# Optimization experiments

Measured on AMD Instinct MI355X. Metric: run time of the kernel, lower is better.

## Reference

```python
import jax, jax.numpy as jnp
import numpy as np

_COUNTS = [256, 192, 128, 64]


def _l2norm(x, axis=1):
    # F.normalize(p=2): x / max(||x||, eps)
    return x / jnp.maximum(jnp.linalg.norm(x, axis=axis, keepdims=True), 1e-12)


def _gcn(x, w1, b1, w2, b2, w3, b3):
    # stack of kernel-size-1 Conv1d == channel matmuls; x: [B, C, N]
    h = jax.nn.relu(jnp.einsum('oc,bcn->bon', w1, x) + b1[:, None])
    h = jax.nn.relu(jnp.einsum('oc,bcn->bon', w2, h) + b2[:, None])
    return jnp.einsum('oc,bcn->bon', w3, h) + b3[:, None]


def setup_inputs() -> dict:
    key = jax.random.key(0)
    ks = iter(jax.random.split(key, 64))
    feat_shapes = [(8, 256, 100, 100), (8, 512, 50, 50), (8, 1024, 25, 25), (8, 2048, 13, 13)]
    chans = [256, 512, 1024, 2048]
    C = 256
    d = {}
    for i, s in enumerate(feat_shapes):
        d[f'feat{i}'] = jax.random.normal(next(ks), s, jnp.float32)
    for i, (ci, ni) in enumerate(zip(chans, _COUNTS)):
        d[f'w_sem_{i}'] = jax.random.normal(next(ks), (ni, ci), jnp.float32) * 0.02
        d[f'w_emb_{i}'] = jax.random.normal(next(ks), (C, ci), jnp.float32) * 0.02
        d[f'w_q_{i}'] = jax.random.normal(next(ks), (C, ci), jnp.float32) * 0.02
        d[f'w_out_{i}'] = jax.random.normal(next(ks), (C, C), jnp.float32) * 0.02
        d[f'w_res_{i}'] = jax.random.normal(next(ks), (C, ci), jnp.float32) * 0.02
    d['gw1'] = jax.random.normal(next(ks), (4, 64, C), jnp.float32) * 0.05
    d['gb1'] = jnp.zeros((4, 64), jnp.float32)
    d['gw2'] = jax.random.normal(next(ks), (4, 64, 64), jnp.float32) * 0.05
    d['gb2'] = jnp.zeros((4, 64), jnp.float32)
    d['gw3'] = jax.random.normal(next(ks), (4, C, 64), jnp.float32) * 0.05
    d['gb3'] = jnp.zeros((4, C), jnp.float32)
    d['mw1'] = jax.random.normal(next(ks), (64, C), jnp.float32) * 0.05
    d['mb1'] = jnp.zeros((64,), jnp.float32)
    d['mw2'] = jax.random.normal(next(ks), (64, 64), jnp.float32) * 0.05
    d['mb2'] = jnp.zeros((64,), jnp.float32)
    d['mw3'] = jax.random.normal(next(ks), (C, 64), jnp.float32) * 0.05
    d['mb3'] = jnp.zeros((C,), jnp.float32)
    return d


def reference(feat0, feat1, feat2, feat3,
              w_sem_0, w_sem_1, w_sem_2, w_sem_3,
              w_emb_0, w_emb_1, w_emb_2, w_emb_3,
              w_q_0, w_q_1, w_q_2, w_q_3,
              w_out_0, w_out_1, w_out_2, w_out_3,
              w_res_0, w_res_1, w_res_2, w_res_3,
              gw1, gb1, gw2, gb2, gw3, gb3,
              mw1, mb1, mw2, mb2, mw3, mb3):
    feats = [feat0, feat1, feat2, feat3]
    w_sem = [w_sem_0, w_sem_1, w_sem_2, w_sem_3]
    w_emb = [w_emb_0, w_emb_1, w_emb_2, w_emb_3]
    w_q = [w_q_0, w_q_1, w_q_2, w_q_3]
    w_out = [w_out_0, w_out_1, w_out_2, w_out_3]
    w_res = [w_res_0, w_res_1, w_res_2, w_res_3]

    # ---- context collector ----
    contexts = []
    for i in range(4):
        f = feats[i]
        B, ci, H, W = f.shape
        hw = H * W
        sem = jnp.einsum('nc,bchw->bnhw', w_sem[i], f)                 # [B, ni, H, W]
        emb = jnp.einsum('oc,bchw->bohw', w_emb[i], f).reshape(B, -1, hw)  # [B, C, HW]
        fn = _l2norm(f, 1).reshape(B, ci, hw)
        en = _l2norm(sem, 1).reshape(B, -1, hw)
        # torch.einsum('bni,bci->bni') sums over c -> entities * sum_c(features)
        sim = en * fn.sum(axis=1, keepdims=True) * jnp.sqrt(jnp.float32(ci))
        attn = jax.nn.softmax(sim, axis=2)                              # softmax over HW
        contexts.append(jnp.einsum('bop,bnp->bon', emb, attn))          # [B, C, ni]

    # ---- graph reasoning ----
    refined = [_gcn(c, gw1[i], gb1[i], gw2[i], gb2[i], gw3[i], gb3[i]) + c
               for i, c in enumerate(contexts)]
    g = jnp.concatenate(refined, axis=2)                                # [B, C, 640]
    g = _gcn(g, mw1, mb1, mw2, mb2, mw3, mb3) + g

    # ---- context distributor ----
    outs = []
    ptr = 0
    for i in range(4):
        f = feats[i]
        B, ci, H, W = f.shape
        hw = H * W
        ni = _COUNTS[i]
        lc = g[:, :, ptr:ptr + ni]                                      # [B, C, ni]
        ptr += ni
        q = jnp.einsum('oc,bchw->bohw', w_q[i], f).reshape(B, -1, hw)   # [B, C, HW]
        scores = jnp.einsum('bop,bon->bpn', _l2norm(q, 1), _l2norm(lc, 1))  # [B, HW, ni]
        aw = jax.nn.softmax(scores, axis=2)                             # softmax over ni
        wc = jnp.einsum('bon,bpn->bop', lc, aw).reshape(B, -1, H, W)    # [B, C, H, W]
        out = jnp.einsum('oc,bchw->bohw', w_out[i], wc) + jnp.einsum('oc,bchw->bohw', w_res[i], f)
        outs.append(out)
    return tuple(outs)
```

## Files before the change

### kernel.cpp

```cpp
#include <hip/hip_runtime.h>
#include <math.h>


#define BB 8
#define CC 256
#define GG 640

typedef __attribute__((ext_vector_type(8))) short short8;
typedef __attribute__((ext_vector_type(4))) float f32x4;

__device__ __forceinline__ unsigned short f2bf(float f) {
    unsigned int u = __float_as_uint(f);
    u += 0x7fffu + ((u >> 16) & 1u);
    return (unsigned short)(u >> 16);
}
__device__ __forceinline__ float bf2f(unsigned short h) {
    return __uint_as_float(((unsigned int)h) << 16);
}
__device__ __forceinline__ float h2f(unsigned short h) {
    union { unsigned short u; _Float16 x; } cv; cv.u = h; return (float)cv.x;
}
__device__ __forceinline__ unsigned short f2h(float f) {
    union { unsigned short u; _Float16 x; } cv; cv.x = (_Float16)f; return cv.u;
}

__device__ __forceinline__ void glds16(const unsigned short* g, unsigned short* l) {
    __builtin_amdgcn_global_load_lds(
        (const __attribute__((address_space(1))) void*)g,
        (__attribute__((address_space(3))) void*)l, 16, 0, 0);
}

__device__ __forceinline__ int swz(int row, int seg) { return seg ^ ((row >> 1) & 3); }

__global__ __launch_bounds__(256) void mfmaGemm(
    const unsigned short* __restrict__ A, long sA, int lda,
    const unsigned short* __restrict__ B, long sB, int ldb,
    const unsigned short* __restrict__ B2p, long sB2, int ldb2, int Kb,
    void* __restrict__ C, long sC, int ldc, long offC,
    int M, int N, int K, int kChunks, int kChunkLen, int mode,
    int gxn, int gym,
    void* __restrict__ C2, long sC2, int ldc2, long offC2, int M1, int mode2)
{
    __shared__ __align__(16) unsigned short As[2][128 * 32];
    __shared__ __align__(16) unsigned short Bs[2][128 * 32];

    const int nb = (int)gridDim.x;
    int orig = (int)blockIdx.x;
    int xcd = orig & 7, idx = orig >> 3;
    int q8 = nb >> 3, r8 = nb & 7;
    int wg = (xcd < r8) ? (xcd * (q8 + 1) + idx)
                        : (r8 * (q8 + 1) + (xcd - r8) * q8 + idx);
    int mb, nbk, z;
    if (N >= M) { mb = wg % gym; int t = wg / gym; nbk = t % gxn; z = t / gxn; }
    else        { nbk = wg % gxn; int t = wg / gxn; mb = t % gym; z = t / gym; }

    const int b = z / kChunks, chunk = z - b * kChunks;
    const int kbeg = chunk * kChunkLen;
    const int kend = min(K, kbeg + kChunkLen);
    const int m0 = mb * 128, n0 = nbk * 128;

    const unsigned short* Ab  = A + (long)b * sA;
    const unsigned short* Bb  = B + (long)b * sB;
    const unsigned short* Bb2 = B2p ? (B2p + (long)b * sB2) : nullptr;

    const int tid = threadIdx.x;
    const int row = tid >> 2, seg = tid & 3;
    const int wave = tid >> 6, lane = tid & 63;
    const int wm = (wave & 1) * 64, wn = (wave >> 1) * 64;
    const int lm = lane & 15, kq = lane >> 4;

    const bool okA  = ((lda  & 7) == 0) && ((((size_t)Ab)  & 15) == 0);
    const bool okB  = ((ldb  & 7) == 0) && ((((size_t)Bb)  & 15) == 0);
    const bool okB2 = Bb2 && ((ldb2 & 7) == 0) && ((((size_t)Bb2) & 15) == 0);

    f32x4 acc[4][4];
    #pragma unroll
    for (int i = 0; i < 4; ++i)
        #pragma unroll
        for (int j = 0; j < 4; ++j) acc[i][j] = (f32x4){0.f, 0.f, 0.f, 0.f};

    auto stageF = [&](const unsigned short* Pb, int ld, int o0,
                      unsigned short* LS, int kg) {
        #pragma unroll
        for (int l = 0; l < 2; ++l) {
            int rf = l * 64 + row;
            const unsigned short* src = Pb + (long)(o0 + rf) * ld + kg + swz(rf, seg) * 8;
            glds16(src, &LS[rf * 32 + seg * 8]);
        }
    };
    auto stageS = [&](const unsigned short* Pb, int ld, int lim, int o0,
                      unsigned short* LS, int kg, int lend) {
        #pragma unroll
        for (int l = 0; l < 2; ++l) {
            int rf = l * 64 + row;
            int kgg = kg + swz(rf, seg) * 8;
            int krem = lend - kgg;
            int g = o0 + rf;
            uint4 v = make_uint4(0u, 0u, 0u, 0u);
            if (g < lim && krem > 0) {
                const unsigned short* src = Pb + (long)g * ld + kgg;
                if (krem >= 8 && ((((size_t)src) & 15) == 0)) {
                    v = *(const uint4*)src;
                } else {
                    __align__(16) unsigned short tmp[8] = {0,0,0,0,0,0,0,0};
                    int c = krem < 8 ? krem : 8;
                    for (int j = 0; j < c; ++j) tmp[j] = src[j];
                    v = *(const uint4*)tmp;
                }
            }
            *(uint4*)&LS[rf * 32 + seg * 8] = v;
        }
    };
    auto stage = [&](int kg, int buf) {
        bool full = (kg + 32 <= kend);
        if (okA && full) stageF(Ab, lda, m0, As[buf], kg);
        else             stageS(Ab, lda, M, m0, As[buf], kg, kend);
        if (kg < Kb) {
            if (okB && full) stageF(Bb, ldb, n0, Bs[buf], kg);
            else             stageS(Bb, ldb, N, n0, Bs[buf], kg, min(kend, Kb));
        } else {
            int kl = kg - Kb;
            if (okB2 && full) stageF(Bb2, ldb2, n0, Bs[buf], kl);
            else              stageS(Bb2, ldb2, N, n0, Bs[buf], kl, kend - Kb);
        }
    };

    stage(kbeg, 0);
    int cur = 0;
    for (int k0 = kbeg; k0 < kend; k0 += 32) {
        __syncthreads();
        if (k0 + 32 < kend) stage(k0 + 32, cur ^ 1);

        short8 af[4], bfr[4];
        #pragma unroll
        for (int mt = 0; mt < 4; ++mt) {
            int rA = wm + mt * 16 + lm;
            af[mt] = *(const short8*)&As[cur][rA * 32 + swz(rA, kq) * 8];
        }
        #pragma unroll
        for (int nt = 0; nt < 4; ++nt) {
            int rB = wn + nt * 16 + lm;
            bfr[nt] = *(const short8*)&Bs[cur][rB * 32 + swz(rB, kq) * 8];
        }
        #pragma unroll
        for (int mt = 0; mt < 4; ++mt)
            #pragma unroll
            for (int nt = 0; nt < 4; ++nt)
                acc[mt][nt] = __builtin_amdgcn_mfma_f32_16x16x32_bf16(
                    af[mt], bfr[nt], acc[mt][nt], 0, 0, 0);
        cur ^= 1;
    }

    const long cb1 = (long)b * sC + offC;
    const long cb2 = (long)b * sC2 + offC2;
    #pragma unroll
    for (int mt = 0; mt < 4; ++mt) {
        #pragma unroll
        for (int nt = 0; nt < 4; ++nt) {
            int n_g = n0 + wn + nt * 16 + lm;
            if (n_g >= N) continue;
            #pragma unroll
            for (int r = 0; r < 4; ++r) {
                int m_g = m0 + wm + mt * 16 + kq * 4 + r;
                if (m_g >= M) continue;
                float v = acc[mt][nt][r];
                void* Cp; int md; long cix;
                if (m_g < M1) { Cp = C;  md = mode;  cix = cb1 + (long)m_g * ldc + n_g; }
                else          { Cp = C2; md = mode2; cix = cb2 + (long)(m_g - M1) * ldc2 + n_g; }
                if (md == 0)      ((float*)Cp)[cix] = v;
                else if (md == 1) ((float*)Cp)[cix] += v;
                else if (md == 2) atomicAdd(&((float*)Cp)[cix], v);
                else if (md == 3) ((unsigned short*)Cp)[cix] = f2h(v);
                else              ((unsigned short*)Cp)[cix] = f2bf(v);
            }
        }
    }
}

__global__ __launch_bounds__(256) void gemmA(
    const float* __restrict__ W, long sW,
    const float* __restrict__ X, long sX, int ldx, long offX,
    float* __restrict__ Cd, long sC, int ldc, long offC,
    const float* __restrict__ bias,
    const float* __restrict__ res, long sR, int ldr, long offR,
    int O, int K, int P, int relu, int accum,
    int lvlFuse, long wStride, int bStride)
{
    __shared__ float Ws[16][64];
    __shared__ float Xs[16][64];
    const int tid = threadIdx.x;
    const int tx = tid & 15;
    const int ty = tid >> 4;
    const int b  = blockIdx.z;
    const int o0 = blockIdx.y * 64;
    const int p0 = blockIdx.x * 64;

    const float* Wp = W;
    const float* bp = bias;
    if (lvlFuse) {
        int lvl = p0 >= 576 ? 3 : p0 >= 448 ? 2 : p0 >= 256 ? 1 : 0;
        Wp += (long)lvl * wStride;
        if (bias) bp += (long)lvl * bStride;
    }
    const float* Wb = Wp + (long)b * sW;
    const float* Xb = X + (long)b * sX + offX;

    float acc[4][4] = {};

    const int wo = tid >> 2;
    const int wk = (tid & 3) * 4;
    const int xp = tid & 63;
    const int xq = tid >> 6;

    for (int k0 = 0; k0 < K; k0 += 16) {
        #pragma unroll
        for (int u = 0; u < 4; ++u) {
            int kk = wk + u;
            float v = 0.f;
            if (o0 + wo < O && k0 + kk < K) v = Wb[(long)(o0 + wo) * K + k0 + kk];
            Ws[kk][wo] = v;
        }
        #pragma unroll
        for (int u = 0; u < 4; ++u) {
            int kk = xq * 4 + u;
            float v = 0.f;
            if (p0 + xp < P && k0 + kk < K) v = Xb[(long)(k0 + kk) * ldx + (p0 + xp)];
            Xs[kk][xp] = v;
        }
        __syncthreads();
        #pragma unroll
        for (int kk = 0; kk < 16; ++kk) {
            float4 wv = *(const float4*)&Ws[kk][ty * 4];
            float4 xv = *(const float4*)&Xs[kk][tx * 4];
            float wa[4] = {wv.x, wv.y, wv.z, wv.w};
            float xa[4] = {xv.x, xv.y, xv.z, xv.w};
            #pragma unroll
            for (int i = 0; i < 4; ++i)
                #pragma unroll
                for (int j = 0; j < 4; ++j)
                    acc[i][j] += wa[i] * xa[j];
        }
        __syncthreads();
    }

    #pragma unroll
    for (int i = 0; i < 4; ++i) {
        int o = o0 + ty * 4 + i;
        if (o >= O) continue;
        #pragma unroll
        for (int j = 0; j < 4; ++j) {
            int p = p0 + tx * 4 + j;
            if (p >= P) continue;
            float v = acc[i][j];
            if (bias) v += bp[o];
            if (relu) v = fmaxf(v, 0.f);
            if (res)  v += res[(long)b * sR + offR + (long)o * ldr + p];
            long ci_ = (long)b * sC + offC + (long)o * ldc + p;
            if (accum) Cd[ci_] += v; else Cd[ci_] = v;
        }
    }
}

__global__ __launch_bounds__(256) void transCvtF(
    const float* __restrict__ src, long sS, int R, int Cc,
    unsigned short* __restrict__ dst, long sD,
    const float* __restrict__ scale, long sScale)
{
    __shared__ float tile[32][33];
    int b = blockIdx.z;
    int r0 = blockIdx.y * 32, c0 = blockIdx.x * 32;
    const float* sb = src + (long)b * sS;
    unsigned short* db = dst + (long)b * sD;
    int tr = threadIdx.x >> 5, tc = threadIdx.x & 31;
    #pragma unroll
    for (int it = 0; it < 4; ++it) {
        int r = r0 + tr + it * 8, c = c0 + tc;
        tile[tr + it * 8][tc] = (r < R && c < Cc) ? sb[(long)r * Cc + c] : 0.f;
    }
    __syncthreads();
    #pragma unroll
    for (int it = 0; it < 4; ++it) {
        int c = c0 + tr + it * 8;
        int r = r0 + tc;
        if (c < Cc && r < R) {
            float v = tile[tc][tr + it * 8];
            if (scale) v *= scale[(long)b * sScale + c];
            db[(long)c * R + r] = f2bf(v);
        }
    }
}

__global__ __launch_bounds__(256) void transCvtH(
    const unsigned short* __restrict__ src, long sS, int R, int Cc,
    unsigned short* __restrict__ dst, long sD,
    const float* __restrict__ scale, long sScale)
{
    __shared__ float tile[32][33];
    int b = blockIdx.z;
    int r0 = blockIdx.y * 32, c0 = blockIdx.x * 32;
    const unsigned short* sb = src + (long)b * sS;
    unsigned short* db = dst + (long)b * sD;
    int tr = threadIdx.x >> 5, tc = threadIdx.x & 31;
    #pragma unroll
    for (int it = 0; it < 4; ++it) {
        int r = r0 + tr + it * 8, c = c0 + tc;
        tile[tr + it * 8][tc] = (r < R && c < Cc) ? h2f(sb[(long)r * Cc + c]) : 0.f;
    }
    __syncthreads();
    #pragma unroll
    for (int it = 0; it < 4; ++it) {
        int c = c0 + tr + it * 8;
        int r = r0 + tc;
        if (c < Cc && r < R) {
            float v = tile[tc][tr + it * 8];
            if (scale) v *= scale[(long)b * sScale + c];
            db[(long)c * R + r] = f2bf(v);
        }
    }
}

__global__ __launch_bounds__(256) void posStatsT(
    const unsigned short* __restrict__ featT, float* __restrict__ fscale,
    int ci, int hw, float sq)
{
    int b = blockIdx.y, p = blockIdx.x;
    const unsigned short* row = featT + ((long)b * hw + p) * ci;
    float s = 0.f, ss = 0.f;
    for (int c = threadIdx.x; c < ci; c += 256) {
        float v = bf2f(row[c]); s += v; ss += v * v;
    }
    __shared__ float rs[256], rss[256];
    int tid = threadIdx.x;
    rs[tid] = s; rss[tid] = ss; __syncthreads();
    for (int st = 128; st > 0; st >>= 1) {
        if (tid < st) { rs[tid] += rs[tid + st]; rss[tid] += rss[tid + st]; }
        __syncthreads();
    }
    if (tid == 0)
        fscale[(long)b * hw + p] = rs[0] / fmaxf(sqrtf(rss[0]), 1e-12f) * sq;
}

__global__ void enScale(const unsigned short* __restrict__ sem, float* __restrict__ fscale,
                        int ni, int hw)
{
    int b = blockIdx.y;
    int p = blockIdx.x * 256 + threadIdx.x;
    if (p >= hw) return;
    const unsigned short* sb = sem + (long)b * ni * hw + p;
    float ss = 0.f;
    for (int n = 0; n < ni; ++n) { float v = h2f(sb[(long)n * hw]); ss += v * v; }
    fscale[(long)b * hw + p] = fscale[(long)b * hw + p] / fmaxf(sqrtf(ss), 1e-12f);
}

__global__ __launch_bounds__(256) void softmaxHW(
    unsigned short* buf, const float* __restrict__ scale, int ni, int hw)
{
    int b = blockIdx.y, n = blockIdx.x;
    unsigned short* row = buf + ((long)b * ni + n) * hw;
    const float* sc = scale + (long)b * hw;
    __shared__ float red[256];
    int tid = threadIdx.x;

    float m = -1e30f;
    for (int p = tid; p < hw; p += 256) m = fmaxf(m, h2f(row[p]) * sc[p]);
    red[tid] = m; __syncthreads();
    for (int s = 128; s > 0; s >>= 1) {
        if (tid < s) red[tid] = fmaxf(red[tid], red[tid + s]);
        __syncthreads();
    }
    m = red[0]; __syncthreads();

    float sum = 0.f;
    for (int p = tid; p < hw; p += 256) sum += __expf(h2f(row[p]) * sc[p] - m);
    red[tid] = sum; __syncthreads();
    for (int s = 128; s > 0; s >>= 1) {
        if (tid < s) red[tid] += red[tid + s];
        __syncthreads();
    }
    float inv = 1.0f / red[0];

    for (int p = tid; p < hw; p += 256) {
        float v = __expf(h2f(row[p]) * sc[p] - m) * inv;
        row[p] = f2bf(v);
    }
}

__global__ void softmaxN(unsigned short* buf, int hw, int ni)
{
    int b = blockIdx.y;
    int wav = threadIdx.x >> 6, lane = threadIdx.x & 63;
    int p = blockIdx.x * 4 + wav;
    if (p >= hw) return;
    unsigned short* row = buf + ((long)b * hw + p) * ni;
    float m = -1e30f;
    for (int n = lane; n < ni; n += 64) m = fmaxf(m, h2f(row[n]));
    for (int off = 32; off > 0; off >>= 1) m = fmaxf(m, __shfl_xor(m, off));
    float s = 0.f;
    for (int n = lane; n < ni; n += 64) s += __expf(h2f(row[n]) - m);
    for (int off = 32; off > 0; off >>= 1) s += __shfl_xor(s, off);
    float inv = 1.f / s;
    for (int n = lane; n < ni; n += 64) {
        float v = __expf(h2f(row[n]) - m) * inv;
        row[n] = f2bf(v);
    }
}

__global__ void lcRnorm(const float* __restrict__ g2, float* __restrict__ lcr)
{
    int b = blockIdx.y;
    int col = blockIdx.x * 256 + threadIdx.x;
    if (col >= GG) return;
    const float* gb = g2 + (long)b * CC * GG + col;
    float ss = 0.f;
    for (int o = 0; o < CC; ++o) { float v = gb[o * GG]; ss += v * v; }
    lcr[b * GG + col] = 1.f / fmaxf(sqrtf(ss), 1e-12f);
}

__global__ void buildLc(const float* __restrict__ g2, const float* __restrict__ lcr,
                        unsigned short* __restrict__ lcnT, unsigned short* __restrict__ lcB,
                        int ni, int ptr)
{
    long t = (long)blockIdx.x * 256 + threadIdx.x;
    if (t >= (long)BB * ni * CC) return;
    int o = (int)(t & (CC - 1));
    long r = t >> 8;
    int n = (int)(r % ni);
    int b = (int)(r / ni);
    float raw = g2[(long)b * CC * GG + (long)o * GG + ptr + n];
    lcnT[t] = f2bf(raw * lcr[b * GG + ptr + n]);
    lcB[((long)b * CC + o) * ni + n] = f2bf(raw);
}

__global__ void qNormCol(const unsigned short* __restrict__ q, float* __restrict__ scl, int hw)
{
    int b = blockIdx.y;
    int p = blockIdx.x * 256 + threadIdx.x;
    if (p >= hw) return;
    const unsigned short* qb = q + (long)b * CC * hw + p;
    float ss = 0.f;
    for (int o = 0; o < CC; ++o) { float v = h2f(qb[(long)o * hw]); ss += v * v; }
    scl[(long)b * hw + p] = 1.f / fmaxf(sqrtf(ss), 1e-12f);
}

struct CvtJob { const float* src; long off; int n; int K; int ld; int colOff; };
struct CvtJobs { CvtJob j[20]; };
__global__ void cvtAllK(CvtJobs jobs, unsigned short* __restrict__ dst)
{
    const CvtJob J = jobs.j[blockIdx.y];
    int t = blockIdx.x * 256 + threadIdx.x;
    if (t < J.n) {
        int r = t / J.K, c = t - r * J.K;
        dst[J.off + (long)r * J.ld + J.colOff + c] = f2bf(J.src[t]);
    }
}

__global__ void cvtOut(const float* __restrict__ src, unsigned short* __restrict__ dst,
                       int n, int toF16)
{
    int i = blockIdx.x * 256 + threadIdx.x;
    if (i >= n) return;
    float v = src[i];
    dst[i] = toF16 ? f2h(v) : f2bf(v);
}

extern "C" void kernel_launch(void* const* d_in, const int* in_sizes, int n_in,
                              void* d_out, int out_size, void* d_ws, size_t ws_size,
                              hipStream_t stream)
{
    (void)n_in; (void)out_size;
    static const int  CI[4]  = {256, 512, 1024, 2048};
    static const int  NI[4]  = {256, 192, 128, 64};
    static const int  HWs[4] = {10000, 2500, 625, 169};
    static const int  PTR[4] = {0, 256, 448, 576};
    static const long OUTOFF[4] = {0, 20480000L, 25600000L, 26880000L};

    const float* feat[4];
    for (int i = 0; i < 4; ++i) feat[i] = (const float*)d_in[i];

    const float *w_sem[4], *w_emb[4], *w_q[4], *w_out[4], *w_res[4];
    bool grouped = (in_sizes[5] == 192 * 512);
    for (int i = 0; i < 4; ++i) {
        if (grouped) {
            w_sem[i] = (const float*)d_in[4 + i];
            w_emb[i] = (const float*)d_in[8 + i];
            w_q[i]   = (const float*)d_in[12 + i];
            w_out[i] = (const float*)d_in[16 + i];
            w_res[i] = (const float*)d_in[20 + i];
        } else {
            int base = 4 + 5 * i;
            w_sem[i] = (const float*)d_in[base + 0];
            w_emb[i] = (const float*)d_in[base + 1];
            w_q[i]   = (const float*)d_in[base + 2];
            w_out[i] = (const float*)d_in[base + 3];
            w_res[i] = (const float*)d_in[base + 4];
        }
    }
    const float* gw1 = (const float*)d_in[24];
    const float* gb1 = (const float*)d_in[25];
    const float* gw2 = (const float*)d_in[26];
    const float* gb2 = (const float*)d_in[27];
    const float* gw3 = (const float*)d_in[28];
    const float* gb3 = (const float*)d_in[29];
    const float* mw1 = (const float*)d_in[30];
    const float* mb1 = (const float*)d_in[31];
    const float* mw2 = (const float*)d_in[32];
    const float* mb2 = (const float*)d_in[33];
    const float* mw3 = (const float*)d_in[34];
    const float* mb3 = (const float*)d_in[35];

    char* wp = (char*)d_ws;
    auto carve = [&](size_t bytes) { char* r = wp; wp += (bytes + 255) & ~(size_t)255; return r; };
    unsigned short* R1 = (unsigned short*)carve(40960000);
    unsigned short* R2 = (unsigned short*)carve(40960000);
    unsigned short* R3 = (unsigned short*)carve(40960000);
    float* ctxg = (float*)carve(5242880);
    float* gbuf = (float*)carve(5242880);
    float* g2   = (float*)carve(5242880);
    float* h1   = (float*)carve(1310720);
    float* h2   = (float*)carve(1310720);
    unsigned short* lcnT = (unsigned short*)carve(1048576);
    unsigned short* lcB  = (unsigned short*)carve(1048576);
    float* lcr  = (float*)carve(20480);
    float* scl  = (float*)carve(320000);
    float* SK   = (float*)carve(5120000);
    unsigned short* wbuf = (unsigned short*)carve(7500000);

    unsigned short* featP[4];
    featP[0] = R1;
    {
        size_t f1 = 2UL * BB * 2500 * 512;
        size_t f2 = 2UL * BB * 625 * 1024;
        size_t f3 = 2UL * BB * 169 * 2048;
        size_t used = (size_t)(wp - (char*)d_ws);
        bool ok = (used + f1 + f2 + f3 + (1u << 20) + 4096) <= ws_size;
        if (ok) {
            featP[1] = (unsigned short*)carve(f1);
            featP[2] = (unsigned short*)carve(f2);
            featP[3] = (unsigned short*)carve(f3);
            carve(1u << 20);
        } else {
            featP[1] = featP[2] = featP[3] = R1;
        }
    }
    bool persist = (featP[1] != R1);

    float* outp = (float*)d_out;

    CvtJobs jobs;
    unsigned short *wsemB[4], *wqB[4], *woutresB[4];
    long woff = 0; int maxn = 0, jx = 0;
    auto addJob = [&](const float* s, int n, int K, int ld, int colOff, long off) {
        jobs.j[jx].src = s; jobs.j[jx].off = off; jobs.j[jx].n = n;
        jobs.j[jx].K = K; jobs.j[jx].ld = ld; jobs.j[jx].colOff = colOff;
        if (n > maxn) maxn = n;
        ++jx;
    };
    for (int i = 0; i < 4; ++i) {
        int ci = CI[i], ni = NI[i];
        wsemB[i] = wbuf + woff;
        addJob(w_sem[i], ni * ci, ci, ci, 0, woff);  woff += ni * ci;
        addJob(w_emb[i], CC * ci, ci, ci, 0, woff);  woff += CC * ci;
        wqB[i] = wbuf + woff;
        addJob(w_q[i],   CC * ci, ci, ci, 0, woff);  woff += CC * ci;
        woutresB[i] = wbuf + woff;
        addJob(w_out[i], CC * CC, CC, CC + ci, 0,  woff);
        addJob(w_res[i], CC * ci, ci, CC + ci, CC, woff);
        woff += (long)CC * (CC + ci);
    }

    cvtAllK<<<dim3((maxn + 255) / 256, 20), 256, 0, stream>>>(jobs, wbuf);

    auto mgFull = [&](const unsigned short* A, long sA, int lda,
                      const unsigned short* B1, long sB1, int ldb1,
                      const unsigned short* B2, long sB2, int ldb2, int Kb,
                      void* Cp, long sC, int ldc, long offC,
                      int M, int N, int K, int mode, int kc,
                      void* C2, long sC2, int ldc2, long offC2, int M1, int mode2) {
        if (kc < 1) kc = 1;
        int kLen = ((K + kc - 1) / kc + 31) & ~31;
        int kcc = (K + kLen - 1) / kLen;
        int gxn = (N + 127) / 128, gym = (M + 127) / 128;
        dim3 g((unsigned)(gxn * gym * BB * kcc));
        mfmaGemm<<<g, 256, 0, stream>>>(A, sA, lda, B1, sB1, ldb1,
                                        B2, sB2, ldb2, Kb,
                                        Cp, sC, ldc, offC, M, N, K, kcc, kLen, mode,
                                        gxn, gym, C2, sC2, ldc2, offC2, M1, mode2);
    };
    auto mg = [&](const unsigned short* A, long sA, int lda,
                  const unsigned short* Bp, long sB, int ldb,
                  void* Cp, long sC, int ldc, long offC,
                  int M, int N, int K, int mode, int kc) {
        mgFull(A, sA, lda, Bp, sB, ldb, nullptr, 0, 8, K,
               Cp, sC, ldc, offC, M, N, K, mode, kc,
               nullptr, 0, 1, 0, M, 0);
    };
    auto projTo = [&](const unsigned short* Wbf, int K, const unsigned short* Xt, long sXt,
                      unsigned short* dst, int M, int N, int fmode) {
        int blocks = ((M + 127) / 128) * ((N + 127) / 128) * BB;
        if (blocks >= 256 || K < 512) {
            mg(Wbf, 0, K, Xt, sXt, K, dst, (long)M * N, N, 0, M, N, K, fmode, 1);
        } else {
            int kc = (256 + blocks - 1) / blocks;
            hipMemsetAsync(SK, 0, (size_t)BB * M * N * 4, stream);
            mg(Wbf, 0, K, Xt, sXt, K, SK, (long)M * N, N, 0, M, N, K, 2, kc);
            long tot = (long)BB * M * N;
            cvtOut<<<dim3((unsigned)((tot + 255) / 256)), 256, 0, stream>>>(
                SK, dst, (int)tot, fmode == 3 ? 1 : 0);
        }
    };

    hipMemsetAsync(ctxg, 0, (size_t)BB * CC * GG * 4, stream);

    for (int i = 0; i < 4; ++i) {
        int ci = CI[i], ni = NI[i], hw = HWs[i];
        unsigned short* fT = featP[i];
        transCvtF<<<dim3((hw + 31) / 32, (ci + 31) / 32, BB), 256, 0, stream>>>(
            feat[i], (long)ci * hw, ci, hw, fT, (long)hw * ci, nullptr, 0);
        posStatsT<<<dim3(hw, BB), 256, 0, stream>>>(fT, scl, ci, hw, sqrtf((float)ci));
        if (i < 2) {
            mgFull(wsemB[i], 0, ci, fT, (long)hw * ci, ci, nullptr, 0, 8, ci,
                   R2, (long)ni * hw, hw, 0,
                   ni + CC, hw, ci, 3, 1,
                   R3, (long)CC * hw, hw, 0, ni, 4);
        } else {
            projTo(wsemB[i], ci, fT, (long)hw * ci, R2, ni, hw, 3);
            projTo(wsemB[i] + (long)ni * ci, ci, fT, (long)hw * ci, R3, CC, hw, 4);
        }
        enScale<<<dim3((hw + 255) / 256, BB), 256, 0, stream>>>(R2, scl, ni, hw);
        softmaxHW<<<dim3(ni, BB), 256, 0, stream>>>(R2, scl, ni, hw);
        {
            int blocks = ((CC + 127) / 128) * ((ni + 127) / 128) * BB;
            int kc = (blocks < 256 && hw >= 512) ? (256 + blocks - 1) / blocks : 1;
            mg(R3, (long)CC * hw, hw, R2, (long)ni * hw, hw,
               ctxg, (long)CC * GG, GG, PTR[i], CC, ni, hw, 2, kc);
        }
    }

    {
        dim3 gl(GG / 64, 1, BB);
        gemmA<<<gl, 256, 0, stream>>>(gw1, 0, ctxg, (long)CC * GG, GG, 0,
                                      h1, (long)64 * GG, GG, 0, gb1,
                                      nullptr, 0, 0, 0, 64, CC, GG, 1, 0,
                                      1, (long)64 * CC, 64);
        gemmA<<<gl, 256, 0, stream>>>(gw2, 0, h1, (long)64 * GG, GG, 0,
                                      h2, (long)64 * GG, GG, 0, gb2,
                                      nullptr, 0, 0, 0, 64, 64, GG, 1, 0,
                                      1, (long)64 * 64, 64);
        dim3 gl2(GG / 64, CC / 64, BB);
        gemmA<<<gl2, 256, 0, stream>>>(gw3, 0, h2, (long)64 * GG, GG, 0,
                                       gbuf, (long)CC * GG, GG, 0, gb3,
                                       ctxg, (long)CC * GG, GG, 0, CC, 64, GG, 0, 0,
                                       1, (long)CC * 64, CC);
    }
    {
        dim3 gl(GG / 64, 1, BB);
        gemmA<<<gl, 256, 0, stream>>>(mw1, 0, gbuf, (long)CC * GG, GG, 0,
                                      h1, (long)64 * GG, GG, 0, mb1,
                                      nullptr, 0, 0, 0, 64, CC, GG, 1, 0, 0, 0, 0);
        gemmA<<<gl, 256, 0, stream>>>(mw2, 0, h1, (long)64 * GG, GG, 0,
                                      h2, (long)64 * GG, GG, 0, mb2,
                                      nullptr, 0, 0, 0, 64, 64, GG, 1, 0, 0, 0, 0);
        dim3 gl2(GG / 64, CC / 64, BB);
        gemmA<<<gl2, 256, 0, stream>>>(mw3, 0, h2, (long)64 * GG, GG, 0,
                                       g2, (long)CC * GG, GG, 0, mb3,
                                       gbuf, (long)CC * GG, GG, 0, CC, 64, GG, 0, 0, 0, 0, 0);
    }

    lcRnorm<<<dim3(3, BB), 256, 0, stream>>>(g2, lcr);

    for (int i = 0; i < 4; ++i) {
        int ci = CI[i], ni = NI[i], hw = HWs[i];
        long tot = (long)BB * ni * CC;
        buildLc<<<dim3((unsigned)((tot + 255) / 256)), 256, 0, stream>>>(
            g2, lcr, lcnT, lcB, ni, PTR[i]);
        unsigned short* fT = featP[i];
        if (!persist)
            transCvtF<<<dim3((hw + 31) / 32, (ci + 31) / 32, BB), 256, 0, stream>>>(
                feat[i], (long)ci * hw, ci, hw, fT, (long)hw * ci, nullptr, 0);
        projTo(wqB[i], ci, fT, (long)hw * ci, R2, CC, hw, 3);
        qNormCol<<<dim3((hw + 255) / 256, BB), 256, 0, stream>>>(R2, scl, hw);
        transCvtH<<<dim3((hw + 31) / 32, (CC + 31) / 32, BB), 256, 0, stream>>>(
            R2, (long)CC * hw, CC, hw, R3, (long)hw * CC, scl, hw);
        mg(R3, (long)hw * CC, CC, lcnT, (long)ni * CC, CC,
           R2, (long)hw * ni, ni, 0, hw, ni, CC, 3, 1);
        softmaxN<<<dim3((hw + 3) / 4, BB), 256, 0, stream>>>(R2, hw, ni);
        mg(R2, (long)hw * ni, ni, lcB, (long)CC * ni, ni,
           R3, (long)hw * CC, CC, 0, hw, CC, ni, 4, 1);
        {
            int K = CC + ci;
            int blocks = ((CC + 127) / 128) * ((hw + 127) / 128) * BB;
            if (blocks >= 256) {
                mgFull(woutresB[i], 0, K, R3, (long)hw * CC, CC,
                       fT, (long)hw * ci, ci, CC,
                       outp, (long)CC * hw, hw, OUTOFF[i], CC, hw, K, 0, 1,
                       nullptr, 0, 1, 0, CC, 0);
            } else {
                int kc = (256 + blocks - 1) / blocks;
                hipMemsetAsync(outp + OUTOFF[i], 0, (size_t)BB * CC * hw * 4, stream);
                mgFull(woutresB[i], 0, K, R3, (long)hw * CC, CC,
                       fT, (long)hw * ci, ci, CC,
                       outp, (long)CC * hw, hw, OUTOFF[i], CC, hw, K, 2, kc,
                       nullptr, 0, 1, 0, CC, 0);
            }
        }
    }
}
```

Measured before the change: 1.984 ms.

## Add triple-buffered LDS pipeline with vmcnt waits to bf16 MFMA GEMM

Adds a three-stage LDS ring buffer for the GEMM's A/B tiles when all operands are aligned and K is a multiple of 32. Loads are issued two k-steps ahead via global_load_lds, and the loop waits with a partial s_waitcnt vmcnt instead of a full __syncthreads. The aim is to hide global-load latency behind MFMA compute. It raises LDS use from 32KB to 48KB per block, which may reduce occupancy. It also relies on hand-counted vmcnt values that must match the number of in-flight loads.

Result: no change. 1.973 ms (-0.6%).

```diff
diff --git a/kernel.cpp b/kernel.cpp
--- a/kernel.cpp
+++ b/kernel.cpp
@@ -41,8 +41,8 @@
     int gxn, int gym,
     void* __restrict__ C2, long sC2, int ldc2, long offC2, int M1, int mode2)
 {
-    __shared__ __align__(16) unsigned short As[2][128 * 32];
-    __shared__ __align__(16) unsigned short Bs[2][128 * 32];
+    __shared__ __align__(16) unsigned short As[3][128 * 32];
+    __shared__ __align__(16) unsigned short Bs[3][128 * 32];
 
     const int nb = (int)gridDim.x;
     int orig = (int)blockIdx.x;
@@ -79,13 +79,21 @@
         #pragma unroll
         for (int j = 0; j < 4; ++j) acc[i][j] = (f32x4){0.f, 0.f, 0.f, 0.f};
 
-    auto stageF = [&](const unsigned short* Pb, int ld, int o0,
-                      unsigned short* LS, int kg) {
+    auto stageP = [&](int kg, int buf) {
         #pragma unroll
         for (int l = 0; l < 2; ++l) {
             int rf = l * 64 + row;
-            const unsigned short* src = Pb + (long)(o0 + rf) * ld + kg + swz(rf, seg) * 8;
-            glds16(src, &LS[rf * 32 + seg * 8]);
+            const unsigned short* src = Ab + (long)(m0 + rf) * lda + kg + swz(rf, seg) * 8;
+            glds16(src, &As[buf][rf * 32 + seg * 8]);
+        }
+        const unsigned short* Pb; int ld; long kg2;
+        if (kg < Kb) { Pb = Bb;  ld = ldb;  kg2 = kg; }
+        else         { Pb = Bb2; ld = ldb2; kg2 = kg - Kb; }
+        #pragma unroll
+        for (int l = 0; l < 2; ++l) {
+            int rf = l * 64 + row;
+            const unsigned short* src = Pb + (long)(n0 + rf) * ld + kg2 + swz(rf, seg) * 8;
+            glds16(src, &Bs[buf][rf * 32 + seg * 8]);
         }
     };
     auto stageS = [&](const unsigned short* Pb, int ld, int lim, int o0,
@@ -113,24 +121,37 @@
     };
     auto stage = [&](int kg, int buf) {
         bool full = (kg + 32 <= kend);
-        if (okA && full) stageF(Ab, lda, m0, As[buf], kg);
-        else             stageS(Ab, lda, M, m0, As[buf], kg, kend);
+        if (okA && full) {
+            #pragma unroll
+            for (int l = 0; l < 2; ++l) {
+                int rf = l * 64 + row;
+                const unsigned short* src = Ab + (long)(m0 + rf) * lda + kg + swz(rf, seg) * 8;
+                glds16(src, &As[buf][rf * 32 + seg * 8]);
+            }
+        } else stageS(Ab, lda, M, m0, As[buf], kg, kend);
         if (kg < Kb) {
-            if (okB && full) stageF(Bb, ldb, n0, Bs[buf], kg);
-            else             stageS(Bb, ldb, N, n0, Bs[buf], kg, min(kend, Kb));
+            if (okB && full && kg + 32 <= Kb) {
+                #pragma unroll
+                for (int l = 0; l < 2; ++l) {
+                    int rf = l * 64 + row;
+                    const unsigned short* src = Bb + (long)(n0 + rf) * ldb + kg + swz(rf, seg) * 8;
+                    glds16(src, &Bs[buf][rf * 32 + seg * 8]);
+                }
+            } else stageS(Bb, ldb, N, n0, Bs[buf], kg, min(kend, Kb));
         } else {
             int kl = kg - Kb;
-            if (okB2 && full) stageF(Bb2, ldb2, n0, Bs[buf], kl);
-            else              stageS(Bb2, ldb2, N, n0, Bs[buf], kl, kend - Kb);
+            if (okB2 && full) {
+                #pragma unroll
+                for (int l = 0; l < 2; ++l) {
+                    int rf = l * 64 + row;
+                    const unsigned short* src = Bb2 + (long)(n0 + rf) * ldb2 + kl + swz(rf, seg) * 8;
+                    glds16(src, &Bs[buf][rf * 32 + seg * 8]);
+                }
+            } else stageS(Bb2, ldb2, N, n0, Bs[buf], kl, kend - Kb);
         }
     };
 
-    stage(kbeg, 0);
-    int cur = 0;
-    for (int k0 = kbeg; k0 < kend; k0 += 32) {
-        __syncthreads();
-        if (k0 + 32 < kend) stage(k0 + 32, cur ^ 1);
-
+    auto compute = [&](int cur) {
         short8 af[4], bfr[4];
         #pragma unroll
         for (int mt = 0; mt < 4; ++mt) {
@@ -148,7 +169,35 @@
             for (int nt = 0; nt < 4; ++nt)
                 acc[mt][nt] = __builtin_amdgcn_mfma_f32_16x16x32_bf16(
                     af[mt], bfr[nt], acc[mt][nt], 0, 0, 0);
-        cur ^= 1;
+    };
+
+    const bool pipe = okA && okB && (B2p == nullptr || okB2) &&
+                      (((kend - kbeg) & 31) == 0) && ((Kb & 31) == 0);
+
+    if (pipe) {
+        stageP(kbeg, 0);
+        if (kbeg + 32 < kend) stageP(kbeg + 32, 1);
+        int cur = 0;
+        for (int k0 = kbeg; k0 < kend; k0 += 32) {
+            if (k0 + 32 < kend) asm volatile("s_waitcnt vmcnt(4)" ::: "memory");
+            else                asm volatile("s_waitcnt vmcnt(0)" ::: "memory");
+            __builtin_amdgcn_s_barrier();
+            if (k0 + 64 < kend) {
+                int nb3 = cur + 2; if (nb3 >= 3) nb3 -= 3;
+                stageP(k0 + 64, nb3);
+            }
+            compute(cur);
+            cur = (cur + 1 == 3) ? 0 : cur + 1;
+        }
+    } else {
+        stage(kbeg, 0);
+        int cur = 0;
+        for (int k0 = kbeg; k0 < kend; k0 += 32) {
+            __syncthreads();
+            if (k0 + 32 < kend) stage(k0 + 32, cur ^ 1);
+            compute(cur);
+            cur ^= 1;
+        }
     }
 
     const long cb1 = (long)b * sC + offC;
```
